# Optimization experiments

Measured on AMD Instinct MI355X. Metric: run time of the kernel, lower is better.

The kernel has to match this reference:

```python
import jax, jax.numpy as jnp
import numpy as np

K = 2  # diffusion order
N, S, D, L, C = 4000, 32, 128, 2, 10
THETA = 0.5


def setup_inputs() -> dict:
    key = jax.random.key(0)
    ks = jax.random.split(key, 16)
    w = 0.05  # weight scale to keep tanh/exp in sane range
    return {
        "A": jax.random.uniform(ks[0], (N, N), dtype=jnp.float32),
        "embs": jax.random.normal(ks[1], (L, S, N, D), dtype=jnp.float32),
        "conv1_w": jax.random.normal(ks[2], (K, D, D), dtype=jnp.float32) * w,
        "conv2_w": jax.random.normal(ks[3], (K, D, D), dtype=jnp.float32) * w,
        "lin_in_w": jax.random.normal(ks[4], (D, D), dtype=jnp.float32) * w,
        "lin_out_w": jax.random.normal(ks[5], (D, 2 * D), dtype=jnp.float32) * w,
        "W_psi": jax.random.normal(ks[6], (2 * D, D), dtype=jnp.float32) * w,
        "b_psi": jax.random.normal(ks[7], (D,), dtype=jnp.float32) * w,
        "ae": jax.random.uniform(ks[8], (N, 1, 1), dtype=jnp.float32),
        "ab": jax.random.uniform(ks[9], (N, 1, 1), dtype=jnp.float32),
        "emb_table": jax.random.uniform(ks[10], (N, D), minval=-0.1, maxval=0.1, dtype=jnp.float32),
        "W_p": jax.random.normal(ks[11], (D, C), dtype=jnp.float32) * w,
        "W_c": jax.random.normal(ks[12], (D, D), dtype=jnp.float32) * w,
    }


def _diffusion(A_tilde, X, W):
    # A_tilde: [N,N] (sym-normalized); X: [N,S,D] (linear in X, so batching over S
    # is identical to the per-timestep loop); W: [K,D,D]
    P_f = A_tilde / A_tilde.sum(axis=1, keepdims=True)
    P_v = A_tilde.T / A_tilde.sum(axis=0, keepdims=True)
    Z = jnp.einsum('mn,nsd->msd', P_f, X) @ W[0]
    P_psi_f, P_psi_v = P_f, P_v
    for k in range(1, K):
        if k < K // 2:
            P_psi_f = P_psi_f @ P_f
            M = P_psi_f
        else:
            P_psi_v = P_psi_v @ P_v
            M = P_psi_v
        Z = Z + jnp.einsum('mn,nsd->msd', M, X) @ W[k]
    return Z


def _attention(context, lin_in_w, lin_out_w, ae, ab):
    # context: [N,S,D]; query is the last timestep, output_len == 1
    q = context[:, -1, :] @ lin_in_w.T                    # [N,D]
    scores = jnp.einsum('nd,nsd->ns', q, context)         # [N,S]
    attw = jax.nn.softmax(scores, axis=-1)                # [N,S]
    mix = attw[:, None, :] * context.transpose(0, 2, 1)   # [N,D,S]
    delta_t = jnp.arange(S - 1, -1, -1, dtype=context.dtype)  # flipped arange
    bt = jnp.exp(-ab * delta_t[None, None, :])            # [N,1,S]
    term2 = jax.nn.relu(ae * mix * bt)                    # [N,D,S]
    mix_sum = (term2 + mix).sum(axis=-1)                  # [N,D]
    combined = jnp.concatenate([mix_sum, q], axis=-1)     # [N,2D]
    return jnp.tanh(combined @ lin_out_w.T)               # [N,D]


def reference(A, embs, conv1_w, conv2_w, lin_in_w, lin_out_w, W_psi, b_psi,
              ae, ab, emb_table, W_p, W_c):
    n = A.shape[0]
    A_t = A + jnp.eye(n, dtype=A.dtype)
    d_inv_sqrt = A_t.sum(axis=1) ** -0.5
    A_tilde = d_inv_sqrt[:, None] * A_t * d_inv_sqrt[None, :]

    outs = []
    for l in range(L):
        X = embs[l].transpose(1, 0, 2)                    # [N,S,D]
        h = _diffusion(A_tilde, X, conv1_w)
        h = jax.nn.relu(h)
        h = _diffusion(A_tilde, h, conv2_w)               # [N,S,D]
        # fusion with theta = 0.5 (h_tilde is the raw embedding)
        fused = jnp.concatenate([THETA * h, (1.0 - THETA) * X], axis=-1) @ W_psi + b_psi
        outs.append(_attention(fused, lin_in_w, lin_out_w, ae, ab))
    outputs = jnp.stack(outs)                             # [L,N,D]

    # embedding lookup over arange(N) is an identity gather
    qs = jax.nn.relu(emb_table)                           # [N,D]
    betas = jnp.exp(jnp.einsum('nd,lne->lde', qs, jnp.tanh(outputs)))  # [L,D,D]
    betas = betas / betas.sum(axis=0)
    Z = jnp.einsum('lnd,lde->ne', outputs, betas)         # [N,D]

    P = jax.nn.softmax(Z @ W_p, axis=1)                   # [N,C]
    C_mat = P.T @ Z                                       # [C,D]
    eta = P.T @ A @ P                                     # [C,C] (vectorized eta_ij)
    C_prime = jax.nn.relu(eta @ (C_mat @ W_c.T))          # [C,D]
    return P @ C_prime                                    # [N,D]
```

## Files before the change

kernel.cpp:

```cpp
#include <hip/hip_runtime.h>
#include <hip/hip_bf16.h>


typedef __attribute__((ext_vector_type(8))) short short8;
typedef __attribute__((ext_vector_type(4))) float f32x4;
typedef __attribute__((ext_vector_type(4))) unsigned short us4;

__device__ __forceinline__ unsigned short f2bf(float x) {
  unsigned int u = __builtin_bit_cast(unsigned int, x);
  u += 0x7FFFu + ((u >> 16) & 1u);
  return (unsigned short)(u >> 16);
}

__device__ __forceinline__ void gload16(const void* g, void* l) {
  __builtin_amdgcn_global_load_lds((const __attribute__((address_space(1))) void*)g,
                                   (__attribute__((address_space(3))) void*)l, 16, 0, 0);
}

__device__ __forceinline__ void barrier_() {
  __builtin_amdgcn_sched_barrier(0);
  asm volatile("" ::: "memory");
  __builtin_amdgcn_s_barrier();
  asm volatile("" ::: "memory");
  __builtin_amdgcn_sched_barrier(0);
}
__device__ __forceinline__ void lgkm0() {
  asm volatile("s_waitcnt lgkmcnt(0)" ::: "memory");
  __builtin_amdgcn_sched_barrier(0);
}

template<int TRANS, int RELU>
__global__ __launch_bounds__(512, 2)
void gemm256(const unsigned short* __restrict__ Ap, int lda,
             const unsigned short* __restrict__ Bp, int ldb,
             unsigned short* __restrict__ outp, int ldo, int K)
{
  __shared__ alignas(16) unsigned short lds[65536];
  const int t = threadIdx.x;
  const int lane = t & 63;
  const int wave = t >> 6;
  const int wm = wave >> 2;
  const int wn = wave & 3;
  const int lrow = lane & 15;
  const int kgrp = lane >> 4;
  const int slotbase = (kgrp ^ (lrow & 7)) << 3;

  const int b = blockIdx.x;
  const int wg = (b & 7) * 32 + (b >> 3);
  const int m0 = (wg >> 4) << 8;
  const int j0 = (wg & 15) << 8;

  const int prow = t >> 3;
  const int lslot = (t & 7) ^ (prow & 7);
  const unsigned short* srcA = Ap + (size_t)(m0 + prow) * lda + lslot * 8;
  const unsigned short* srcB = Bp + (size_t)(j0 + prow) * ldb + lslot * 8;
  const size_t a64 = (size_t)64 * lda, a128 = (size_t)128 * lda;
  const size_t b64 = (size_t)64 * ldb, b128 = (size_t)128 * ldb;
  unsigned short* dA = &lds[t * 8];
  unsigned short* dB = &lds[16384 + t * 8];
  const int NT = K >> 6;

#define STG_A(h, kb, kt) { const unsigned short* s_ = srcA + (h)*a128 + (size_t)(kt)*64; \
    gload16(s_, dA + (kb)*32768 + (h)*8192); \
    gload16(s_ + a64, dA + (kb)*32768 + (h)*8192 + 4096); }
#define STG_B(h, kb, kt) { const unsigned short* s_ = srcB + (h)*b128 + (size_t)(kt)*64; \
    gload16(s_, dB + (kb)*32768 + (h)*8192); \
    gload16(s_ + b64, dB + (kb)*32768 + (h)*8192 + 4096); }

  const int arb = wm * 8192 + lrow * 64 + slotbase;
  const int brb = 16384 + (wn >> 1) * 8192 + ((wn & 1) << 12) + lrow * 64 + slotbase;

#define RD_A(dst, base_off) \
  _Pragma("unroll") for (int mf_ = 0; mf_ < 4; ++mf_) { \
    dst[mf_][0] = *(const short8*)&lds[(base_off) + mf_*1024]; \
    dst[mf_][1] = *(const short8*)&lds[((base_off) ^ 32) + mf_*1024]; }
#define RD_B(dst, base_off) \
  _Pragma("unroll") for (int nf_ = 0; nf_ < 2; ++nf_) { \
    dst[nf_][0] = *(const short8*)&lds[(base_off) + nf_*1024]; \
    dst[nf_][1] = *(const short8*)&lds[((base_off) ^ 32) + nf_*1024]; }

#define MFMA16(AF, BF, MB, NB) \
  _Pragma("unroll") for (int mf_ = 0; mf_ < 4; ++mf_) \
  _Pragma("unroll") for (int nf_ = 0; nf_ < 2; ++nf_) { \
    acc[(MB)+mf_][(NB)+nf_] = __builtin_amdgcn_mfma_f32_16x16x32_bf16(AF[mf_][0], BF[nf_][0], acc[(MB)+mf_][(NB)+nf_], 0,0,0); \
    acc[(MB)+mf_][(NB)+nf_] = __builtin_amdgcn_mfma_f32_16x16x32_bf16(AF[mf_][1], BF[nf_][1], acc[(MB)+mf_][(NB)+nf_], 0,0,0); }

  f32x4 acc[8][4];
#pragma unroll
  for (int i = 0; i < 8; ++i)
#pragma unroll
    for (int j = 0; j < 4; ++j) acc[i][j] = f32x4{0.f, 0.f, 0.f, 0.f};

  short8 a0[4][2], a1[4][2], bv[2][2];

  STG_A(0, 0, 0); STG_A(1, 0, 0); STG_B(0, 0, 0); STG_B(1, 0, 0);
  STG_A(0, 1, 1); STG_A(1, 1, 1);
  asm volatile("s_waitcnt vmcnt(4)" ::: "memory");
  barrier_();

  for (int V = 0; V < NT; ++V) {
    const int cb = (V & 1) << 15;
    RD_A(a0, cb + arb);
    RD_B(bv, cb + brb);
    if (V + 1 < NT) STG_B(0, ((V + 1) & 1), V + 1);
    barrier_(); lgkm0();
    __builtin_amdgcn_s_setprio(1);
    MFMA16(a0, bv, 0, 0);
    __builtin_amdgcn_s_setprio(0);
    barrier_();
    RD_A(a1, cb + arb + 4096);
    if (V + 1 < NT) STG_B(1, ((V + 1) & 1), V + 1);
    barrier_(); lgkm0();
    __builtin_amdgcn_s_setprio(1);
    MFMA16(a1, bv, 4, 0);
    __builtin_amdgcn_s_setprio(0);
    barrier_();
    RD_B(bv, cb + brb + 2048);
    if (V + 2 < NT) STG_A(0, (V & 1), V + 2);
    barrier_(); lgkm0();
    __builtin_amdgcn_s_setprio(1);
    MFMA16(a1, bv, 4, 2);
    __builtin_amdgcn_s_setprio(0);
    barrier_();
    if (V + 2 < NT) STG_A(1, (V & 1), V + 2);
    if (V < NT - 2)       { asm volatile("s_waitcnt vmcnt(4)" ::: "memory"); }
    else if (V == NT - 2) { asm volatile("s_waitcnt vmcnt(0)" ::: "memory"); }
    barrier_();
    __builtin_amdgcn_s_setprio(1);
    MFMA16(a0, bv, 0, 2);
    __builtin_amdgcn_s_setprio(0);
  }

#pragma unroll
  for (int mf = 0; mf < 8; ++mf) {
#pragma unroll
    for (int nf = 0; nf < 4; ++nf) {
      const int m = m0 + wm * 128 + mf * 16 + kgrp * 4;
      const int j = j0 + wn * 64 + nf * 16 + lrow;
      if (TRANS) {
        us4 pk;
#pragma unroll
        for (int r = 0; r < 4; ++r) pk[r] = f2bf(acc[mf][nf][r]);
        *(us4*)(outp + (size_t)j * ldo + m) = pk;
      } else {
#pragma unroll
        for (int r = 0; r < 4; ++r) {
          float v = acc[mf][nf][r];
          if (RELU) v = fmaxf(v, 0.f);
          outp[(size_t)(m + r) * ldo + j] = f2bf(v);
        }
      }
    }
  }
#undef STG_A
#undef STG_B
#undef RD_A
#undef RD_B
#undef MFMA16
}

template<int EPI, int RELU, int BIAS>
__global__ __launch_bounds__(256)
void gemm_nt(const unsigned short* __restrict__ A1,
             const unsigned short* __restrict__ A2,
             int k_switch, int a_zstride, int lda,
             const unsigned short* __restrict__ B, int ldb,
             void* __restrict__ outp,
             long o_j, long o_m, long o_z, long o_jt,
             const float* __restrict__ bias, int K)
{
  __shared__ alignas(16) unsigned short At[128*32];
  __shared__ alignas(16) unsigned short Bt[128*32];
  const int t = threadIdx.x;
  const int lane = t & 63;
  const int wave = t >> 6;
  const int m0 = blockIdx.x << 7;
  const int jt = blockIdx.y;
  const int j0 = jt << 7;
  const int z  = blockIdx.z;
  const int wm = (wave >> 1) << 6;
  const int wn = (wave & 1) << 6;
  const int lrow = lane & 15;
  const int kgrp = lane >> 4;

  const unsigned short* A1z = A1 + (long)z * a_zstride;
  const unsigned short* A2z = A2 + (long)z * a_zstride;

  f32x4 acc[4][4];
#pragma unroll
  for (int i = 0; i < 4; ++i)
#pragma unroll
    for (int j = 0; j < 4; ++j) acc[i][j] = f32x4{0.f, 0.f, 0.f, 0.f};

  const int r0 = t >> 2, q0 = t & 3;
  const int c1 = t + 256;
  const int r1 = c1 >> 2, q1 = c1 & 3;

  for (int k0 = 0; k0 < K; k0 += 32) {
    const unsigned short* As; int ka;
    if (k0 < k_switch) { As = A1z; ka = k0; } else { As = A2z; ka = k0 - k_switch; }
    gload16(As + (long)(m0 + r0) * lda + ka + q0 * 8, At + t * 8);
    gload16(As + (long)(m0 + r1) * lda + ka + q1 * 8, At + c1 * 8);
    gload16(B  + (long)(j0 + r0) * ldb + k0 + q0 * 8, Bt + t * 8);
    gload16(B  + (long)(j0 + r1) * ldb + k0 + q1 * 8, Bt + c1 * 8);
    __syncthreads();
    short8 af[4], bv[4];
#pragma unroll
    for (int i = 0; i < 4; ++i)
      af[i] = *(const short8*)(At + (wm + i * 16 + lrow) * 32 + kgrp * 8);
#pragma unroll
    for (int i = 0; i < 4; ++i)
      bv[i] = *(const short8*)(Bt + (wn + i * 16 + lrow) * 32 + kgrp * 8);
#pragma unroll
    for (int i = 0; i < 4; ++i)
#pragma unroll
      for (int j = 0; j < 4; ++j)
        acc[i][j] = __builtin_amdgcn_mfma_f32_16x16x32_bf16(af[i], bv[j], acc[i][j], 0, 0, 0);
    __syncthreads();
  }

  const int mlb = wm + kgrp * 4;
#pragma unroll
  for (int i = 0; i < 4; ++i) {
#pragma unroll
    for (int j = 0; j < 4; ++j) {
      const int jl = wn + j * 16 + lrow;
      const int ml = mlb + i * 16;
      if (EPI == 0) {
        long base = (long)jl * o_j + (long)(m0 + ml) * o_m + (long)z * o_z + (long)jt * o_jt;
        us4 pk;
#pragma unroll
        for (int r = 0; r < 4; ++r) pk[r] = f2bf(acc[i][j][r]);
        *(us4*)((unsigned short*)outp + base) = pk;
      } else {
        float* of = (float*)outp;
        float badd = BIAS ? bias[j0 + jl] : 0.f;
#pragma unroll
        for (int r = 0; r < 4; ++r) {
          long idx = (long)jl * o_j + (long)(m0 + ml + r) * o_m + (long)z * o_z + (long)jt * o_jt;
          of[idx] = acc[i][j][r] + badd;
        }
      }
    }
  }
}

__global__ __launch_bounds__(256) void rowsum_dis(const float* __restrict__ A,
                                                  float* __restrict__ dis) {
  int m = blockIdx.x;
  if (m >= 4000) { if (threadIdx.x == 0) dis[m] = 0.f; return; }
  const float* r = A + (long)m * 4000;
  float a = 0.f;
  for (int i = threadIdx.x; i < 1000; i += 256) {
    float4 v = ((const float4*)r)[i];
    a += v.x + v.y + v.z + v.w;
  }
  for (int o = 32; o; o >>= 1) a += __shfl_xor(a, o);
  __shared__ float ls[4];
  if ((threadIdx.x & 63) == 0) ls[threadIdx.x >> 6] = a;
  __syncthreads();
  if (threadIdx.x == 0) dis[m] = rsqrtf(1.f + ls[0] + ls[1] + ls[2] + ls[3]);
}

__global__ __launch_bounds__(256) void wrow_kernel(const float* __restrict__ A,
                                                   const float* __restrict__ dis,
                                                   float* __restrict__ iwrow) {
  int m = blockIdx.x;
  if (m >= 4000) { if (threadIdx.x == 0) iwrow[m] = 0.f; return; }
  const float* r = A + (long)m * 4000;
  float a = 0.f;
  for (int n = threadIdx.x; n < 4000; n += 256) a += r[n] * dis[n];
  for (int o = 32; o; o >>= 1) a += __shfl_xor(a, o);
  __shared__ float ls[4];
  if ((threadIdx.x & 63) == 0) ls[threadIdx.x >> 6] = a;
  __syncthreads();
  if (threadIdx.x == 0) iwrow[m] = 1.f / (ls[0] + ls[1] + ls[2] + ls[3] + dis[m]);
}

__global__ __launch_bounds__(256) void wcol_part(const float* __restrict__ A,
                                                 const float* __restrict__ dis,
                                                 float* __restrict__ part) {
  int j = blockIdx.x * 256 + threadIdx.x;
  int mz = blockIdx.y;
  float a = 0.f;
  if (j < 4000) {
    int ms = mz * 125;
    for (int m = ms; m < ms + 125; ++m) a += A[(long)m * 4000 + j] * dis[m];
  }
  part[(long)mz * 4096 + j] = a;
}

__global__ __launch_bounds__(256) void wcol_fin(const float* __restrict__ part,
                                                const float* __restrict__ dis,
                                                float* __restrict__ iwcol) {
  int j = blockIdx.x * 256 + threadIdx.x;
  float s = 0.f;
  for (int z = 0; z < 32; ++z) s += part[(long)z * 4096 + j];
  iwcol[j] = (j < 4000) ? 1.f / (s + dis[j]) : 0.f;
}

__global__ __launch_bounds__(256) void build_P(const float* __restrict__ A,
                                               const float* __restrict__ dis,
                                               const float* __restrict__ iwrow,
                                               const float* __restrict__ iwcol,
                                               unsigned short* __restrict__ Pcat,
                                               unsigned short* __restrict__ PV,
                                               unsigned short* __restrict__ PVT) {
  __shared__ float tile[64][65];
  int m0 = blockIdx.y * 64, n0 = blockIdx.x * 64;
#pragma unroll
  for (int i = 0; i < 16; ++i) {
    int idx = i * 256 + threadIdx.x;
    int lr = idx >> 6, lc = idx & 63;
    int m = m0 + lr, n = n0 + lc;
    float v = 0.f;
    if (m < 4000 && n < 4000) {
      float a = A[(long)m * 4000 + n];
      if (m == n) a += 1.f;
      v = a * dis[n];
    }
    Pcat[(long)m * 8192 + n] = f2bf(v * iwrow[m]);
    float pv = v * iwcol[m];
    PVT[(long)m * 4096 + n] = f2bf(pv);
    tile[lr][lc] = pv;
  }
  __syncthreads();
#pragma unroll
  for (int i = 0; i < 16; ++i) {
    int idx = i * 256 + threadIdx.x;
    int lr = idx >> 6, lc = idx & 63;
    PV[(long)(n0 + lr) * 4096 + (m0 + lc)] = f2bf(tile[lc][lr]);
  }
}

__global__ __launch_bounds__(256) void prep_weights(const float* __restrict__ lin_in,
                                                    const float* __restrict__ lin_out,
                                                    const float* __restrict__ c1,
                                                    const float* __restrict__ c2,
                                                    const float* __restrict__ wpsi,
                                                    float* __restrict__ LWiT, float* __restrict__ LWoT,
                                                    unsigned short* __restrict__ CW1T,
                                                    unsigned short* __restrict__ CW2T,
                                                    unsigned short* __restrict__ WPST) {
  int i = blockIdx.x * 256 + threadIdx.x;
  if (i < 16384) {
    int e = i >> 7, d = i & 127;
    LWiT[e * 128 + d] = lin_in[d * 128 + e];
  } else if (i < 49152) {
    int k = i - 16384; int ii = k >> 7, d = k & 127;
    LWoT[k] = lin_out[d * 256 + ii];
  } else if (i < 81920) {
    int k = i - 49152; int j = k >> 7, kk = k & 127;
    CW1T[k] = f2bf(c1[(j >> 7) * 16384 + kk * 128 + (j & 127)]);
  } else if (i < 114688) {
    int k = i - 81920; int j = k >> 7, kk = k & 127;
    CW2T[k] = f2bf(c2[(j >> 7) * 16384 + kk * 128 + (j & 127)]);
  } else if (i < 147456) {
    int k = i - 114688; int e = k >> 8, d2 = k & 255;
    WPST[k] = f2bf(0.5f * wpsi[d2 * 128 + e]);
  }
}

__global__ __launch_bounds__(256) void convert_X(const float* __restrict__ embsL,
                                                 unsigned short* __restrict__ X) {
  long i4 = (long)blockIdx.x * 256 + threadIdx.x;
  long e = i4 << 2;
  int n = (int)(e >> 12);
  int r = (int)(e & 4095);
  us4 o;
  if (n < 4000) {
    int s = r >> 7, d = r & 127;
    float4 v = *(const float4*)(embsL + ((long)s * 4000 + n) * 128 + d);
    o[0] = f2bf(v.x); o[1] = f2bf(v.y); o[2] = f2bf(v.z); o[3] = f2bf(v.w);
  } else { o[0] = o[1] = o[2] = o[3] = 0; }
  *(us4*)(X + (long)n * 4096 + r) = o;
}

__global__ __launch_bounds__(128) void attention_kernel(const float* __restrict__ F,
                                                        const float* __restrict__ LWiT,
                                                        const float* __restrict__ LWoT,
                                                        const float* __restrict__ ae,
                                                        const float* __restrict__ ab,
                                                        float* __restrict__ outp) {
  int n = blockIdx.x, t = threadIdx.x;
  __shared__ float Fs[32 * 132];
  __shared__ float qv[128], msum[128], attw[32], btv[32];
  const float* Fr = F + (long)n * 4096;
  for (int i = t; i < 4096; i += 128) { int s = i >> 7, d = i & 127; Fs[s * 132 + d] = Fr[i]; }
  __syncthreads();
  {
    float a = 0.f;
    const float* Frow = Fs + 31 * 132;
    for (int e = 0; e < 128; ++e) a += Frow[e] * LWiT[e * 128 + t];
    qv[t] = a;
  }
  __syncthreads();
  if (t < 32) {
    float sc = 0.f;
    for (int d = 0; d < 128; ++d) sc += qv[d] * Fs[t * 132 + d];
    float mx = sc;
    for (int o = 16; o; o >>= 1) mx = fmaxf(mx, __shfl_xor(mx, o, 32));
    float ex = expf(sc - mx), sm = ex;
    for (int o = 16; o; o >>= 1) sm += __shfl_xor(sm, o, 32);
    attw[t] = ex / sm;
  } else if (t >= 64 && t < 96) {
    int s = t - 64;
    btv[s] = expf(-ab[n] * (float)(31 - s));
  }
  __syncthreads();
  {
    float aen = ae[n], acc = 0.f;
    for (int s = 0; s < 32; ++s) {
      float f = Fs[s * 132 + t];
      acc += attw[s] * (f + aen * btv[s] * fmaxf(f, 0.f));
    }
    msum[t] = acc;
  }
  __syncthreads();
  {
    float a = 0.f;
    for (int e = 0; e < 128; ++e) a += msum[e] * LWoT[e * 128 + t];
    for (int e = 0; e < 128; ++e) a += qv[e] * LWoT[(e + 128) * 128 + t];
    outp[(long)n * 128 + t] = tanhf(a);
  }
}

__global__ __launch_bounds__(256) void tanh_qs(const float* __restrict__ outs,
                                               const float* __restrict__ embt,
                                               float* __restrict__ T, float* __restrict__ qs) {
  long i = (long)blockIdx.x * 256 + threadIdx.x;
  if (i < 1024000) T[i] = tanhf(outs[i]);
  else { long j = i - 1024000; if (j < 512000) qs[j] = fmaxf(embt[j], 0.f); }
}

__global__ __launch_bounds__(256) void betas_raw_kernel(const float* __restrict__ qs,
                                                        const float* __restrict__ T,
                                                        float* __restrict__ braw) {
  int e = threadIdx.x & 127, dl = threadIdx.x >> 7;
  int d = blockIdx.x * 2 + dl, l = blockIdx.y;
  const float* Tl = T + (long)l * 512000;
  float acc = 0.f;
  for (int n = 0; n < 4000; ++n) acc += qs[(long)n * 128 + d] * Tl[(long)n * 128 + e];
  braw[((long)l * 128 + d) * 128 + e] = acc;
}

__global__ __launch_bounds__(256) void bnorm_kernel(const float* __restrict__ braw,
                                                    float* __restrict__ bn) {
  int i = blockIdx.x * 256 + threadIdx.x;
  float b0 = expf(braw[i]), b1 = expf(braw[16384 + i]);
  float s = b0 + b1;
  bn[i] = b0 / s;
  bn[16384 + i] = b1 / s;
}

__global__ __launch_bounds__(256) void z_kernel(const float* __restrict__ outs,
                                                const float* __restrict__ bn,
                                                float* __restrict__ Zb) {
  int n = blockIdx.x * 2 + (threadIdx.x >> 7);
  int e = threadIdx.x & 127;
  float acc = 0.f;
  for (int l = 0; l < 2; ++l) {
    const float* orow = outs + ((long)l * 4000 + n) * 128;
    const float* brow = bn + (long)l * 16384;
    for (int d = 0; d < 128; ++d) acc += orow[d] * brow[d * 128 + e];
  }
  Zb[(long)n * 128 + e] = acc;
}

__global__ __launch_bounds__(256) void p_kernel(const float* __restrict__ Zb,
                                                const float* __restrict__ Wp,
                                                float* __restrict__ P) {
  int n = blockIdx.x * 4 + (threadIdx.x >> 6);
  int c = threadIdx.x & 63;
  float val = 0.f;
  if (c < 10) {
    const float* zr = Zb + (long)n * 128;
    for (int d = 0; d < 128; ++d) val += zr[d] * Wp[d * 10 + c];
  }
  float mx = val;
  for (int i = 0; i < 10; ++i) mx = fmaxf(mx, __shfl(val, i, 64));
  float ex = (c < 10) ? expf(val - mx) : 0.f;
  float sm = 0.f;
  for (int i = 0; i < 10; ++i) sm += __shfl(ex, i, 64);
  if (c < 12) P[(long)n * 12 + c] = (c < 10) ? ex / sm : 0.f;
}

__global__ __launch_bounds__(256) void ap_kernel(const float* __restrict__ A,
                                                 const float* __restrict__ P,
                                                 float* __restrict__ AP) {
  int m = blockIdx.x, t = threadIdx.x;
  const float* Ar = A + (long)m * 4000;
  float acc[10];
#pragma unroll
  for (int c = 0; c < 10; ++c) acc[c] = 0.f;
  for (int n = t; n < 4000; n += 256) {
    float a = Ar[n];
    const float* Pr = P + (long)n * 12;
#pragma unroll
    for (int c = 0; c < 10; ++c) acc[c] += a * Pr[c];
  }
#pragma unroll
  for (int c = 0; c < 10; ++c)
    for (int o = 32; o; o >>= 1) acc[c] += __shfl_xor(acc[c], o);
  __shared__ float ls[4][10];
  if ((t & 63) == 0)
    for (int c = 0; c < 10; ++c) ls[t >> 6][c] = acc[c];
  __syncthreads();
  if (t < 10) AP[(long)m * 12 + t] = ls[0][t] + ls[1][t] + ls[2][t] + ls[3][t];
  if (t >= 10 && t < 12) AP[(long)m * 12 + t] = 0.f;
}

__global__ __launch_bounds__(256) void etacm_part(const float* __restrict__ P,
                                                  const float* __restrict__ AP,
                                                  const float* __restrict__ Z,
                                                  float* __restrict__ peta,
                                                  float* __restrict__ pcm) {
  int b = blockIdx.x, t = threadIdx.x;
  int ms = b * 63, me = ms + 63; if (me > 4000) me = 4000;
  int i_ = t / 10, j_ = t % 10;
  float ea = 0.f;
  float ca[5];
#pragma unroll
  for (int k = 0; k < 5; ++k) ca[k] = 0.f;
  for (int m = ms; m < me; ++m) {
    if (t < 100) ea += P[(long)m * 12 + i_] * AP[(long)m * 12 + j_];
#pragma unroll
    for (int k = 0; k < 5; ++k) {
      int idx = t + 256 * k;
      int c = idx >> 7, e = idx & 127;
      ca[k] += P[(long)m * 12 + c] * Z[(long)m * 128 + e];
    }
  }
  if (t < 100) peta[(long)b * 100 + t] = ea;
#pragma unroll
  for (int k = 0; k < 5; ++k) pcm[(long)b * 1280 + t + 256 * k] = ca[k];
}

__global__ __launch_bounds__(256) void final_small(const float* __restrict__ peta,
                                                   const float* __restrict__ pcm,
                                                   const float* __restrict__ Wc,
                                                   float* __restrict__ cprime) {
  __shared__ float eta_s[100], cm_s[1280], tmp_s[1280];
  int t = threadIdx.x;
  if (t < 100) {
    float s = 0.f;
    for (int b = 0; b < 64; ++b) s += peta[(long)b * 100 + t];
    eta_s[t] = s;
  }
  for (int i = t; i < 1280; i += 256) {
    float s = 0.f;
    for (int b = 0; b < 64; ++b) s += pcm[(long)b * 1280 + i];
    cm_s[i] = s;
  }
  __syncthreads();
  for (int i = t; i < 1280; i += 256) {
    int c = i >> 7, d = i & 127;
    float s = 0.f;
    for (int e = 0; e < 128; ++e) s += cm_s[c * 128 + e] * Wc[d * 128 + e];
    tmp_s[i] = s;
  }
  __syncthreads();
  for (int i = t; i < 1280; i += 256) {
    int c = i >> 7, d = i & 127;
    float s = 0.f;
    for (int j = 0; j < 10; ++j) s += eta_s[c * 10 + j] * tmp_s[j * 128 + d];
    cprime[i] = fmaxf(s, 0.f);
  }
}

__global__ __launch_bounds__(256) void out_kernel(const float* __restrict__ P,
                                                  const float* __restrict__ cpr,
                                                  float* __restrict__ out) {
  int idx = blockIdx.x * 256 + threadIdx.x;
  int n = idx >> 7, d = idx & 127;
  float s = 0.f;
#pragma unroll
  for (int c = 0; c < 10; ++c) s += P[(long)n * 12 + c] * cpr[c * 128 + d];
  out[idx] = s;
}

extern "C" void kernel_launch(void* const* d_in, const int* in_sizes, int n_in,
                              void* d_out, int out_size, void* d_ws, size_t ws_size,
                              hipStream_t stream) {
  (void)in_sizes; (void)n_in; (void)out_size; (void)ws_size;
  const float* A      = (const float*)d_in[0];
  const float* embs   = (const float*)d_in[1];
  const float* conv1w = (const float*)d_in[2];
  const float* conv2w = (const float*)d_in[3];
  const float* lin_in = (const float*)d_in[4];
  const float* lin_out= (const float*)d_in[5];
  const float* Wpsi   = (const float*)d_in[6];
  const float* bpsi   = (const float*)d_in[7];
  const float* ae     = (const float*)d_in[8];
  const float* ab     = (const float*)d_in[9];
  const float* embt   = (const float*)d_in[10];
  const float* Wp     = (const float*)d_in[11];
  const float* Wc     = (const float*)d_in[12];
  float* out = (float*)d_out;
  char* ws = (char*)d_ws;

  size_t off = 0;
  auto alloc = [&](size_t b) { size_t r = off; off += (b + 255) & ~(size_t)255; return r; };
  unsigned short* PCAT = (unsigned short*)(ws + alloc((size_t)4096 * 8192 * 2));
  char*           BTF  = ws + alloc((size_t)4096 * 8192 * 2);
  unsigned short* BT   = (unsigned short*)BTF;
  float*          Ff   = (float*)BTF;
  unsigned short* XBF  = (unsigned short*)(ws + alloc((size_t)4096 * 4096 * 2));
  unsigned short* PV   = XBF;
  unsigned short* HBUF = (unsigned short*)(ws + alloc((size_t)4096 * 4096 * 2));
  unsigned short* PVT  = HBUF;
  float* DIS   = (float*)(ws + alloc(4096 * 4));
  float* IWROW = (float*)(ws + alloc(4096 * 4));
  float* IWCOL = (float*)(ws + alloc(4096 * 4));
  float* WCP   = (float*)(ws + alloc((size_t)32 * 4096 * 4));
  float* LWIT  = (float*)(ws + alloc(16384 * 4));
  float* LWOT  = (float*)(ws + alloc(32768 * 4));
  unsigned short* CW1T = (unsigned short*)(ws + alloc(32768 * 2));
  unsigned short* CW2T = (unsigned short*)(ws + alloc(32768 * 2));
  unsigned short* WPST = (unsigned short*)(ws + alloc(32768 * 2));
  float* OUTS = (float*)(ws + alloc((size_t)2 * 4000 * 128 * 4));
  float* TT   = (float*)(ws + alloc((size_t)2 * 4000 * 128 * 4));
  float* QS   = (float*)(ws + alloc((size_t)4000 * 128 * 4));
  float* BRAW = (float*)(ws + alloc(32768 * 4));
  float* BNRM = (float*)(ws + alloc(32768 * 4));
  float* ZB   = (float*)(ws + alloc((size_t)4000 * 128 * 4));
  float* PP   = (float*)(ws + alloc((size_t)4000 * 12 * 4));
  float* APB  = (float*)(ws + alloc((size_t)4000 * 12 * 4));
  float* PETA = (float*)(ws + alloc((size_t)64 * 100 * 4));
  float* PCM  = (float*)(ws + alloc((size_t)64 * 1280 * 4));
  float* CPR  = (float*)(ws + alloc(1280 * 4));

  const int BIG = 1 << 30;

  rowsum_dis<<<4096, 256, 0, stream>>>(A, DIS);
  wrow_kernel<<<4096, 256, 0, stream>>>(A, DIS, IWROW);
  wcol_part<<<dim3(16, 32), 256, 0, stream>>>(A, DIS, WCP);
  wcol_fin<<<16, 256, 0, stream>>>(WCP, DIS, IWCOL);
  prep_weights<<<576, 256, 0, stream>>>(lin_in, lin_out, conv1w, conv2w, Wpsi,
                                        LWIT, LWOT, CW1T, CW2T, WPST);
  build_P<<<dim3(64, 64), 256, 0, stream>>>(A, DIS, IWROW, IWCOL, PCAT, PV, PVT);

  gemm256<1, 0><<<256, 512, 0, stream>>>(PVT, 4096, PV, 4096, PCAT + 4096, 8192, 4096);

  for (int l = 0; l < 2; ++l) {
    convert_X<<<16384, 256, 0, stream>>>(embs + (long)l * 32 * 4000 * 128, XBF);
    gemm_nt<0, 0, 0><<<dim3(32, 2, 32), 256, 0, stream>>>(
        XBF, XBF, BIG, 128, 4096, CW1T, 128,
        BT, 8192L, 1L, 128L * 8192, 4096L, nullptr, 128);
    gemm256<0, 1><<<256, 512, 0, stream>>>(PCAT, 8192, BT, 8192, HBUF, 4096, 8192);
    gemm_nt<0, 0, 0><<<dim3(32, 2, 32), 256, 0, stream>>>(
        HBUF, HBUF, BIG, 128, 4096, CW2T, 128,
        BT, 8192L, 1L, 128L * 8192, 4096L, nullptr, 128);
    gemm256<0, 0><<<256, 512, 0, stream>>>(PCAT, 8192, BT, 8192, HBUF, 4096, 8192);
    gemm_nt<2, 0, 1><<<dim3(32, 1, 32), 256, 0, stream>>>(
        HBUF, XBF, 128, 128, 4096, WPST, 256,
        Ff, 1L, 4096L, 128L, 0L, bpsi, 256);
    attention_kernel<<<4000, 128, 0, stream>>>(Ff, LWIT, LWOT, ae, ab,
                                               OUTS + (long)l * 512000);
  }

  tanh_qs<<<6000, 256, 0, stream>>>(OUTS, embt, TT, QS);
  betas_raw_kernel<<<dim3(64, 2), 256, 0, stream>>>(QS, TT, BRAW);
  bnorm_kernel<<<64, 256, 0, stream>>>(BRAW, BNRM);
  z_kernel<<<2000, 256, 0, stream>>>(OUTS, BNRM, ZB);
  p_kernel<<<1000, 256, 0, stream>>>(ZB, Wp, PP);
  ap_kernel<<<4000, 256, 0, stream>>>(A, PP, APB);
  etacm_part<<<64, 256, 0, stream>>>(PP, APB, ZB, PETA, PCM);
  final_small<<<1, 256, 0, stream>>>(PETA, PCM, Wc, CPR);
  out_kernel<<<2000, 256, 0, stream>>>(PP, CPR, out);
}
```

Measured before the change: 1.548 ms.

## Triple-buffer B tiles in LDS to prefetch two k-steps ahead

```diff
diff --git a/kernel.cpp b/kernel.cpp
--- a/kernel.cpp
+++ b/kernel.cpp
@@ -35,7 +35,7 @@
              const unsigned short* __restrict__ Bp, int ldb,
              unsigned short* __restrict__ outp, int ldo, int K)
 {
-  __shared__ alignas(16) unsigned short lds[65536];
+  __shared__ alignas(16) unsigned short lds[81920];
   const int t = threadIdx.x;
   const int lane = t & 63;
   const int wave = t >> 6;
@@ -57,18 +57,18 @@
   const size_t a64 = (size_t)64 * lda, a128 = (size_t)128 * lda;
   const size_t b64 = (size_t)64 * ldb, b128 = (size_t)128 * ldb;
   unsigned short* dA = &lds[t * 8];
-  unsigned short* dB = &lds[16384 + t * 8];
+  unsigned short* dB = &lds[32768 + t * 8];
   const int NT = K >> 6;
 
 #define STG_A(h, kb, kt) { const unsigned short* s_ = srcA + (h)*a128 + (size_t)(kt)*64; \
-    gload16(s_, dA + (kb)*32768 + (h)*8192); \
-    gload16(s_ + a64, dA + (kb)*32768 + (h)*8192 + 4096); }
-#define STG_B(h, kb, kt) { const unsigned short* s_ = srcB + (h)*b128 + (size_t)(kt)*64; \
-    gload16(s_, dB + (kb)*32768 + (h)*8192); \
-    gload16(s_ + b64, dB + (kb)*32768 + (h)*8192 + 4096); }
+    gload16(s_, dA + (kb)*16384 + (h)*8192); \
+    gload16(s_ + a64, dA + (kb)*16384 + (h)*8192 + 4096); }
+#define STG_B(h, bb, kt) { const unsigned short* s_ = srcB + (h)*b128 + (size_t)(kt)*64; \
+    gload16(s_, dB + (bb)*16384 + (h)*8192); \
+    gload16(s_ + b64, dB + (bb)*16384 + (h)*8192 + 4096); }
 
   const int arb = wm * 8192 + lrow * 64 + slotbase;
-  const int brb = 16384 + (wn >> 1) * 8192 + ((wn & 1) << 12) + lrow * 64 + slotbase;
+  const int brb = 32768 + (wn >> 1) * 8192 + ((wn & 1) << 12) + lrow * 64 + slotbase;
 
 #define RD_A(dst, base_off) \
   _Pragma("unroll") for (int mf_ = 0; mf_ < 4; ++mf_) { \
@@ -94,41 +94,46 @@
   short8 a0[4][2], a1[4][2], bv[2][2];
 
   STG_A(0, 0, 0); STG_A(1, 0, 0); STG_B(0, 0, 0); STG_B(1, 0, 0);
-  STG_A(0, 1, 1); STG_A(1, 1, 1);
-  asm volatile("s_waitcnt vmcnt(4)" ::: "memory");
+  STG_A(0, 1, 1); STG_A(1, 1, 1); STG_B(0, 1, 1); STG_B(1, 1, 1);
+  asm volatile("s_waitcnt vmcnt(8)" ::: "memory");
   barrier_();
 
+  int rb3 = 0, sb3 = 2;
   for (int V = 0; V < NT; ++V) {
-    const int cb = (V & 1) << 15;
-    RD_A(a0, cb + arb);
-    RD_B(bv, cb + brb);
-    if (V + 1 < NT) STG_B(0, ((V + 1) & 1), V + 1);
+    const int ab = (V & 1) << 14;
+    const int bb = rb3 << 14;
+    const bool stg = (V + 2 < NT);
+    RD_A(a0, ab + arb);
+    RD_B(bv, bb + brb);
+    if (stg) STG_B(0, sb3, V + 2);
     barrier_(); lgkm0();
     __builtin_amdgcn_s_setprio(1);
     MFMA16(a0, bv, 0, 0);
     __builtin_amdgcn_s_setprio(0);
     barrier_();
-    RD_A(a1, cb + arb + 4096);
-    if (V + 1 < NT) STG_B(1, ((V + 1) & 1), V + 1);
+    RD_A(a1, ab + arb + 4096);
+    if (stg) STG_B(1, sb3, V + 2);
     barrier_(); lgkm0();
     __builtin_amdgcn_s_setprio(1);
     MFMA16(a1, bv, 4, 0);
     __builtin_amdgcn_s_setprio(0);
     barrier_();
-    RD_B(bv, cb + brb + 2048);
-    if (V + 2 < NT) STG_A(0, (V & 1), V + 2);
+    RD_B(bv, bb + brb + 2048);
+    if (stg) STG_A(0, (V & 1), V + 2);
     barrier_(); lgkm0();
     __builtin_amdgcn_s_setprio(1);
     MFMA16(a1, bv, 4, 2);
     __builtin_amdgcn_s_setprio(0);
     barrier_();
-    if (V + 2 < NT) STG_A(1, (V & 1), V + 2);
-    if (V < NT - 2)       { asm volatile("s_waitcnt vmcnt(4)" ::: "memory"); }
-    else if (V == NT - 2) { asm volatile("s_waitcnt vmcnt(0)" ::: "memory"); }
-    barrier_();
+    if (stg) STG_A(1, (V & 1), V + 2);
     __builtin_amdgcn_s_setprio(1);
     MFMA16(a0, bv, 0, 2);
     __builtin_amdgcn_s_setprio(0);
+    if (stg)             { asm volatile("s_waitcnt vmcnt(8)" ::: "memory"); }
+    else if (V + 1 < NT) { asm volatile("s_waitcnt vmcnt(0)" ::: "memory"); }
+    barrier_();
+    rb3 = (rb3 == 2) ? 0 : rb3 + 1;
+    sb3 = (sb3 == 2) ? 0 : sb3 + 1;
   }
 
 #pragma unroll
```

Result: slower. 1.583 ms (+2.2%).
